# Optimization experiments

Measured on AMD Instinct MI355X. Metric: run time of the kernel, lower is better.

The kernel has to match this reference:

```python
import jax, jax.numpy as jnp
import numpy as np

N, C, T, V = 64, 64, 256, 25
R, O = C // 8, 64  # rel_channels, out_channels
ALPHA = 1.0


def setup_inputs() -> dict:
    key = jax.random.key(0)
    ks = jax.random.split(key, 10)
    s = 0.05
    return {
        "x": jax.random.normal(ks[0], (N, C, T, V), dtype=jnp.float32),
        "A": jax.random.normal(ks[1], (V, V), dtype=jnp.float32),
        "w1": jax.random.normal(ks[2], (R, C), dtype=jnp.float32) * s,
        "b1": jnp.zeros((R,), dtype=jnp.float32),
        "w2": jax.random.normal(ks[3], (R, C), dtype=jnp.float32) * s,
        "b2": jnp.zeros((R,), dtype=jnp.float32),
        "w3": jax.random.normal(ks[4], (O, C), dtype=jnp.float32) * s,
        "b3": jnp.zeros((O,), dtype=jnp.float32),
        "w4": jax.random.normal(ks[5], (O, R), dtype=jnp.float32) * s,
        "b4": jnp.zeros((O,), dtype=jnp.float32),
    }


def reference(x, A, w1, b1, w2, b2, w3, b3, w4, b4):
    # x: (N, C, T, V)
    # conv1/conv2 are 1x1 convs followed by mean over T -> (N, R, V)
    x1 = jnp.einsum('nctv,rc->nrv', x, w1) / x.shape[2] + b1[:, None]
    x2 = jnp.einsum('nctv,rc->nrv', x, w2) / x.shape[2] + b2[:, None]
    # conv3: 1x1 conv -> (N, O, T, V)
    x3 = jnp.einsum('nctv,oc->notv', x, w3) + b3[:, None, None]
    # outer-difference attention over joints: (N, R, V, V)
    att = jnp.tanh(x1[:, :, :, None] - x2[:, :, None, :])
    # conv4 channel mix (R->O), scale, add adjacency: (N, O, V, V)
    m = jnp.einsum('nruv,or->nouv', att, w4) + b4[:, None, None]
    m = m * ALPHA + A[None, None, :, :]
    # aggregation: einsum('ncuv,nctv->nctu')
    out = jnp.einsum('ncuv,nctv->nctu', m, x3)
    return out
```

## Files before the change

kernel.cpp:

```cpp
#include <hip/hip_runtime.h>

#define NN 64
#define CC 64
#define TT 256
#define VV 25
#define RR 8
#define OO 64
#define PLANE 6400

__global__ __launch_bounds__(256) void k_xsum(const float* __restrict__ x,
                                              float* __restrict__ xsum) {
  int nc = blockIdx.x;
  const float* src = x + (size_t)nc * PLANE;
  __shared__ float s[PLANE];
  int tid = threadIdx.x;
#pragma unroll
  for (int k = 0; k < 25; ++k) s[k * 256 + tid] = src[k * 256 + tid];
  __syncthreads();
  if (tid < VV) {
    float a0 = 0.f, a1 = 0.f, a2 = 0.f, a3 = 0.f;
    for (int t = 0; t < TT; t += 4) {
      a0 += s[(t + 0) * VV + tid];
      a1 += s[(t + 1) * VV + tid];
      a2 += s[(t + 2) * VV + tid];
      a3 += s[(t + 3) * VV + tid];
    }
    xsum[nc * VV + tid] = (a0 + a1) + (a2 + a3);
  }
}

__global__ void k_wt(const float* __restrict__ w3, float* __restrict__ w3t) {
  int k = blockIdx.x * 256 + threadIdx.x;
  if (k < 4096) {
    int c = k >> 6, o = k & 63;
    w3t[k] = w3[o * 64 + c];
  }
}

__global__ __launch_bounds__(256) void k_build_m(
    const float* __restrict__ xsum, const float* __restrict__ A,
    const float* __restrict__ w1, const float* __restrict__ b1,
    const float* __restrict__ w2, const float* __restrict__ b2,
    const float* __restrict__ w4, const float* __restrict__ b4,
    float* __restrict__ mp) {
  int n = blockIdx.x;
  __shared__ float xs[CC * VV];
  __shared__ float sx1[RR * VV];
  __shared__ float sx2[RR * VV];
  __shared__ float att[RR * 625];
  int tid = threadIdx.x;
  const float* xsn = xsum + n * (CC * VV);
  for (int k = tid; k < CC * VV; k += 256) xs[k] = xsn[k];
  __syncthreads();
  if (tid < RR * VV) {
    int r = tid / VV, v = tid % VV;
    float a1 = 0.f, a2 = 0.f;
#pragma unroll
    for (int c = 0; c < CC; ++c) {
      float xv = xs[c * VV + v];
      a1 = fmaf(w1[r * CC + c], xv, a1);
      a2 = fmaf(w2[r * CC + c], xv, a2);
    }
    sx1[tid] = a1 * (1.f / 256.f) + b1[r];
    sx2[tid] = a2 * (1.f / 256.f) + b2[r];
  }
  __syncthreads();
  for (int k = tid; k < RR * 625; k += 256) {
    int r = k / 625, uv = k % 625;
    int u = uv / VV, v = uv % VV;
    att[k] = tanhf(sx1[r * VV + u] - sx2[r * VV + v]);
  }
  __syncthreads();
  for (int k = tid; k < OO * 625; k += 256) {
    int o = k / 625, uv = k % 625;
    int u = uv / VV, v = uv % VV;
    float a = b4[o] + A[uv];
#pragma unroll
    for (int r = 0; r < RR; ++r) a = fmaf(w4[o * RR + r], att[r * 625 + uv], a);
    mp[(((size_t)n * OO + o) * VV + u) * 32 + v] = a;
  }
}

__global__ __launch_bounds__(256) void k_conv3(const float* __restrict__ x,
                                               const float* __restrict__ w3t,
                                               const float* __restrict__ b3,
                                               float* __restrict__ x3) {
  int n = blockIdx.y;
  int p = blockIdx.x * 256 + threadIdx.x;
  const float* xn = x + (size_t)n * CC * PLANE;
  float acc[OO];
#pragma unroll
  for (int o = 0; o < OO; ++o) acc[o] = b3[o];
#pragma unroll 2
  for (int c = 0; c < CC; ++c) {
    float xv = xn[(size_t)c * PLANE + p];
    const float* w = w3t + c * OO;
#pragma unroll
    for (int o = 0; o < OO; ++o) acc[o] = fmaf(w[o], xv, acc[o]);
  }
  float* dst = x3 + (size_t)n * OO * PLANE + p;
#pragma unroll
  for (int o = 0; o < OO; ++o) dst[(size_t)o * PLANE] = acc[o];
}

__global__ __launch_bounds__(256) void k_aggr(float* __restrict__ out,
                                              const float* __restrict__ mp) {
  int no = blockIdx.x;
  float* base = out + (size_t)no * PLANE;
  __shared__ float s[PLANE];
  int tid = threadIdx.x;
#pragma unroll
  for (int k = 0; k < 25; ++k) s[k * 256 + tid] = base[k * 256 + tid];
  __syncthreads();
  const float* m = mp + (size_t)no * (VV * 32);
  float xr[VV], orow[VV];
#pragma unroll
  for (int v = 0; v < VV; ++v) xr[v] = s[tid * VV + v];
#pragma unroll
  for (int u = 0; u < VV; ++u) {
    float a = 0.f;
#pragma unroll
    for (int v = 0; v < VV; ++v) a = fmaf(m[u * 32 + v], xr[v], a);
    orow[u] = a;
  }
#pragma unroll
  for (int u = 0; u < VV; ++u) s[tid * VV + u] = orow[u];
  __syncthreads();
#pragma unroll
  for (int k = 0; k < 25; ++k) base[k * 256 + tid] = s[k * 256 + tid];
}

extern "C" void kernel_launch(void* const* d_in, const int* in_sizes, int n_in,
                              void* d_out, int out_size, void* d_ws,
                              size_t ws_size, hipStream_t stream) {
  const float* x = (const float*)d_in[0];
  const float* A = (const float*)d_in[1];
  const float* w1 = (const float*)d_in[2];
  const float* b1 = (const float*)d_in[3];
  const float* w2 = (const float*)d_in[4];
  const float* b2 = (const float*)d_in[5];
  const float* w3 = (const float*)d_in[6];
  const float* b3 = (const float*)d_in[7];
  const float* w4 = (const float*)d_in[8];
  const float* b4 = (const float*)d_in[9];
  float* out = (float*)d_out;
  float* ws = (float*)d_ws;

  float* xsum = ws;
  float* w3t = ws + 102400;
  float* mp = ws + 106496;

  k_xsum<<<NN * CC, 256, 0, stream>>>(x, xsum);
  k_wt<<<16, 256, 0, stream>>>(w3, w3t);
  k_build_m<<<NN, 256, 0, stream>>>(xsum, A, w1, b1, w2, b2, w4, b4, mp);
  k_conv3<<<dim3(PLANE / 256, NN), 256, 0, stream>>>(x, w3t, b3, out);
  k_aggr<<<NN * OO, 256, 0, stream>>>(out, mp);
}
```

Measured before the change: 305.7 us.

## Fuse conv3 and aggregation into one MFMA bf16 kernel with bf16 transposed input

Replaces the xsum, weight transpose, fp32 conv3 and aggregation kernels with a prep kernel that converts x to a channel-last bf16 layout and computes partial T-sums, then a fused kernel that runs conv3 on bf16 MFMA into LDS and applies the per-channel VxV aggregation before writing output. The aim is to avoid writing and rereading the full fp32 x3 intermediate through global memory and to move the 1x1 conv onto matrix cores. The cost is bf16 rounding of x, w3 and x3, and extra bf16 workspace traffic. The fused kernel launches only 256 blocks of 512 threads with large LDS, so occupancy is low.

Result: slower. 339.0 us (+10.9%).

```diff
diff --git a/kernel.cpp b/kernel.cpp
--- a/kernel.cpp
+++ b/kernel.cpp
@@ -8,40 +8,73 @@
 #define OO 64
 #define PLANE 6400
 
-__global__ __launch_bounds__(256) void k_xsum(const float* __restrict__ x,
-                                              float* __restrict__ xsum) {
-  int nc = blockIdx.x;
-  const float* src = x + (size_t)nc * PLANE;
-  __shared__ float s[PLANE];
+typedef __attribute__((ext_vector_type(8))) short short8;
+typedef __attribute__((ext_vector_type(4))) float f32x4;
+
+__device__ inline unsigned short f2bf(float f) {
+  unsigned int u = __builtin_bit_cast(unsigned int, f);
+  u = u + 0x7fffu + ((u >> 16) & 1u);
+  return (unsigned short)(u >> 16);
+}
+__device__ inline float bf2f(unsigned short h) {
+  unsigned int u = ((unsigned int)h) << 16;
+  return __builtin_bit_cast(float, u);
+}
+
+__global__ __launch_bounds__(512) void k_prep(const float* __restrict__ x,
+                                              unsigned short* __restrict__ xbf,
+                                              float* __restrict__ part) {
+  int pt = blockIdx.x;
+  int n = blockIdx.y;
   int tid = threadIdx.x;
-#pragma unroll
-  for (int k = 0; k < 25; ++k) s[k * 256 + tid] = src[k * 256 + tid];
-  __syncthreads();
-  if (tid < VV) {
-    float a0 = 0.f, a1 = 0.f, a2 = 0.f, a3 = 0.f;
-    for (int t = 0; t < TT; t += 4) {
-      a0 += s[(t + 0) * VV + tid];
-      a1 += s[(t + 1) * VV + tid];
-      a2 += s[(t + 2) * VV + tid];
-      a3 += s[(t + 3) * VV + tid];
-    }
-    xsum[nc * VV + tid] = (a0 + a1) + (a2 + a3);
-  }
-}
-
-__global__ void k_wt(const float* __restrict__ w3, float* __restrict__ w3t) {
-  int k = blockIdx.x * 256 + threadIdx.x;
-  if (k < 4096) {
-    int c = k >> 6, o = k & 63;
-    w3t[k] = w3[o * 64 + c];
+  __shared__ unsigned short s[800 * 66];
+  const float* xn = x + (size_t)n * CC * PLANE + pt * 800;
+#pragma unroll 1
+  for (int i = 0; i < 25; ++i) {
+    int idx4 = i * 512 + tid;
+    int c = idx4 / 200;
+    int p4 = (idx4 - c * 200) * 4;
+    const float4 v = *(const float4*)(xn + (size_t)c * PLANE + p4);
+    s[(p4 + 0) * 66 + c] = f2bf(v.x);
+    s[(p4 + 1) * 66 + c] = f2bf(v.y);
+    s[(p4 + 2) * 66 + c] = f2bf(v.z);
+    s[(p4 + 3) * 66 + c] = f2bf(v.w);
+  }
+  __syncthreads();
+#pragma unroll 1
+  for (int i = 0; i < 4; ++i) {
+    int idx = i * 512 + tid;
+    if (idx < 1600) {
+      int c = idx / 25, v = idx - c * 25;
+      float a = 0.f;
+#pragma unroll
+      for (int t = 0; t < 32; ++t) a += bf2f(s[(t * 25 + v) * 66 + c]);
+      part[((size_t)n * 8 + pt) * 1600 + idx] = a;
+    }
+  }
+  unsigned int* dst = (unsigned int*)(xbf + ((size_t)n * PLANE + pt * 800) * 64);
+#pragma unroll 1
+  for (int i = 0; i < 13; ++i) {
+    int idx = i * 512 + tid;
+    if (idx < 6400) {
+      int p = idx >> 3, ch = idx & 7;
+      const unsigned int* sp = (const unsigned int*)(s + p * 66 + ch * 8);
+      uint4 val;
+      val.x = sp[0];
+      val.y = sp[1];
+      val.z = sp[2];
+      val.w = sp[3];
+      *(uint4*)(dst + (size_t)idx * 4) = val;
+    }
   }
 }
 
 __global__ __launch_bounds__(256) void k_build_m(
-    const float* __restrict__ xsum, const float* __restrict__ A,
+    const float* __restrict__ part, const float* __restrict__ A,
     const float* __restrict__ w1, const float* __restrict__ b1,
     const float* __restrict__ w2, const float* __restrict__ b2,
     const float* __restrict__ w4, const float* __restrict__ b4,
+    const float* __restrict__ w3, unsigned short* __restrict__ w3bf,
     float* __restrict__ mp) {
   int n = blockIdx.x;
   __shared__ float xs[CC * VV];
@@ -49,8 +82,13 @@
   __shared__ float sx2[RR * VV];
   __shared__ float att[RR * 625];
   int tid = threadIdx.x;
-  const float* xsn = xsum + n * (CC * VV);
-  for (int k = tid; k < CC * VV; k += 256) xs[k] = xsn[k];
+  for (int k = tid; k < OO * CC; k += 256) w3bf[k] = f2bf(w3[k]);
+  for (int k = tid; k < CC * VV; k += 256) {
+    float a = 0.f;
+#pragma unroll
+    for (int pt = 0; pt < 8; ++pt) a += part[((size_t)n * 8 + pt) * 1600 + k];
+    xs[k] = a;
+  }
   __syncthreads();
   if (tid < RR * VV) {
     int r = tid / VV, v = tid % VV;
@@ -77,57 +115,78 @@
     float a = b4[o] + A[uv];
 #pragma unroll
     for (int r = 0; r < RR; ++r) a = fmaf(w4[o * RR + r], att[r * 625 + uv], a);
-    mp[(((size_t)n * OO + o) * VV + u) * 32 + v] = a;
-  }
-}
-
-__global__ __launch_bounds__(256) void k_conv3(const float* __restrict__ x,
-                                               const float* __restrict__ w3t,
-                                               const float* __restrict__ b3,
-                                               float* __restrict__ x3) {
+    mp[((size_t)(n * OO + o) * VV + u) * 32 + v] = a;
+  }
+}
+
+__global__ __launch_bounds__(512, 1) void k_fused(
+    const unsigned short* __restrict__ xbf,
+    const unsigned short* __restrict__ w3bf, const float* __restrict__ b3,
+    const float* __restrict__ mp, float* __restrict__ out) {
+  int ttile = blockIdx.x;
   int n = blockIdx.y;
-  int p = blockIdx.x * 256 + threadIdx.x;
-  const float* xn = x + (size_t)n * CC * PLANE;
-  float acc[OO];
-#pragma unroll
-  for (int o = 0; o < OO; ++o) acc[o] = b3[o];
-#pragma unroll 2
-  for (int c = 0; c < CC; ++c) {
-    float xv = xn[(size_t)c * PLANE + p];
-    const float* w = w3t + c * OO;
-#pragma unroll
-    for (int o = 0; o < OO; ++o) acc[o] = fmaf(w[o], xv, acc[o]);
-  }
-  float* dst = x3 + (size_t)n * OO * PLANE + p;
-#pragma unroll
-  for (int o = 0; o < OO; ++o) dst[(size_t)o * PLANE] = acc[o];
-}
-
-__global__ __launch_bounds__(256) void k_aggr(float* __restrict__ out,
-                                              const float* __restrict__ mp) {
-  int no = blockIdx.x;
-  float* base = out + (size_t)no * PLANE;
-  __shared__ float s[PLANE];
   int tid = threadIdx.x;
-#pragma unroll
-  for (int k = 0; k < 25; ++k) s[k * 256 + tid] = base[k * 256 + tid];
-  __syncthreads();
-  const float* m = mp + (size_t)no * (VV * 32);
-  float xr[VV], orow[VV];
-#pragma unroll
-  for (int v = 0; v < VV; ++v) xr[v] = s[tid * VV + v];
-#pragma unroll
-  for (int u = 0; u < VV; ++u) {
-    float a = 0.f;
-#pragma unroll
-    for (int v = 0; v < VV; ++v) a = fmaf(m[u * 32 + v], xr[v], a);
-    orow[u] = a;
-  }
-#pragma unroll
-  for (int u = 0; u < VV; ++u) s[tid * VV + u] = orow[u];
-  __syncthreads();
-#pragma unroll
-  for (int k = 0; k < 25; ++k) base[k * 256 + tid] = s[k * 256 + tid];
+  int lane = tid & 63, wave = tid >> 6;
+  int l15 = lane & 15, q = lane >> 4;
+  __shared__ unsigned short x3s[32 * 1602];
+  __shared__ float tbuf[8][1600];
+  const unsigned short* xbn = xbf + ((size_t)n * PLANE + ttile * 1600) * 64;
+
+#pragma unroll 1
+  for (int chunk = 0; chunk < 2; ++chunk) {
+    short8 afr[2][2];
+#pragma unroll
+    for (int ot = 0; ot < 2; ++ot)
+#pragma unroll
+      for (int q2 = 0; q2 < 2; ++q2)
+        afr[ot][q2] = *(const short8*)(w3bf + (chunk * 32 + ot * 16 + l15) * 64 +
+                                       q2 * 32 + q * 8);
+#pragma unroll 1
+    for (int i = 0; i < 13; ++i) {
+      int pt = i * 8 + wave;
+      if (pt < 100) {
+        const unsigned short* bp = xbn + (size_t)(pt * 16 + l15) * 64 + q * 8;
+        short8 b0 = *(const short8*)(bp);
+        short8 b1 = *(const short8*)(bp + 32);
+        int p_loc = pt * 16 + l15;
+#pragma unroll
+        for (int ot = 0; ot < 2; ++ot) {
+          f32x4 d = {0.f, 0.f, 0.f, 0.f};
+          d = __builtin_amdgcn_mfma_f32_16x16x32_bf16(afr[ot][0], b0, d, 0, 0, 0);
+          d = __builtin_amdgcn_mfma_f32_16x16x32_bf16(afr[ot][1], b1, d, 0, 0, 0);
+          int orow = ot * 16 + q * 4;
+#pragma unroll
+          for (int r = 0; r < 4; ++r)
+            x3s[(orow + r) * 1602 + p_loc] = f2bf(d[r]);
+        }
+      }
+    }
+    __syncthreads();
+#pragma unroll 1
+    for (int j = 0; j < 4; ++j) {
+      int ol = wave * 4 + j;
+      int o = __builtin_amdgcn_readfirstlane(chunk * 32 + ol);
+      const float* mrow = mp + ((size_t)(n * OO + o) * VV) * 32;
+      float b3o = b3[o];
+      int t = lane;
+      float xr[VV];
+#pragma unroll
+      for (int v = 0; v < VV; ++v)
+        xr[v] = bf2f(x3s[ol * 1602 + t * 25 + v]) + b3o;
+      float* tb = tbuf[wave];
+#pragma unroll
+      for (int u = 0; u < VV; ++u) {
+        float a = 0.f;
+#pragma unroll
+        for (int v = 0; v < VV; ++v) a = fmaf(mrow[u * 32 + v], xr[v], a);
+        tb[t * 25 + u] = a;
+      }
+      float* op = out + ((size_t)(n * OO + o) * TT + ttile * 64) * VV;
+#pragma unroll
+      for (int k = 0; k < 25; ++k) op[k * 64 + lane] = tb[k * 64 + lane];
+    }
+    __syncthreads();
+  }
 }
 
 extern "C" void kernel_launch(void* const* d_in, const int* in_sizes, int n_in,
@@ -144,15 +203,15 @@
   const float* w4 = (const float*)d_in[8];
   const float* b4 = (const float*)d_in[9];
   float* out = (float*)d_out;
-  float* ws = (float*)d_ws;
-
-  float* xsum = ws;
-  float* w3t = ws + 102400;
-  float* mp = ws + 106496;
-
-  k_xsum<<<NN * CC, 256, 0, stream>>>(x, xsum);
-  k_wt<<<16, 256, 0, stream>>>(w3, w3t);
-  k_build_m<<<NN, 256, 0, stream>>>(xsum, A, w1, b1, w2, b2, w4, b4, mp);
-  k_conv3<<<dim3(PLANE / 256, NN), 256, 0, stream>>>(x, w3t, b3, out);
-  k_aggr<<<NN * OO, 256, 0, stream>>>(out, mp);
-}
+  char* ws = (char*)d_ws;
+
+  unsigned short* xbf = (unsigned short*)ws;
+  float* part = (float*)(ws + 52428800);
+  float* mp = (float*)(ws + 55705600);
+  unsigned short* w3bf = (unsigned short*)(ws + 68812800);
+
+  k_prep<<<dim3(8, NN), 512, 0, stream>>>(x, xbf, part);
+  k_build_m<<<NN, 256, 0, stream>>>(part, A, w1, b1, w2, b2, w4, b4, w3, w3bf,
+                                    mp);
+  k_fused<<<dim3(4, NN), 512, 0, stream>>>(xbf, w3bf, b3, mp, out);
+}
```
